# Performance work log

Measured on AMD Instinct MI355X. Metric: run time of the kernel, lower is better.

Reference implementation:

```python
import jax, jax.numpy as jnp
import numpy as np

N_NODES = 50000


def _gin_aggregate(x, src, dst):
    # sum_{j in N(i)} x_j via scatter-add over edges; eps=0 so add self term
    msg = x[src]  # [E, d]
    return x + jax.ops.segment_sum(msg, dst, num_segments=N_NODES)


def _mlp(h, Wa, ba, Wb, bb):
    return jax.nn.relu(h @ Wa + ba) @ Wb + bb


def setup_inputs() -> dict:
    key = jax.random.key(0)
    ks = jax.random.split(key, 12)
    d_in, d_h, n_cls, n_edges = 128, 128, 40, 800000
    x = jax.random.normal(ks[0], (N_NODES, d_in), dtype=jnp.float32)
    edge_index = jax.random.randint(ks[1], (2, n_edges), 0, N_NODES, dtype=jnp.int64)
    s = lambda k, sh: jax.random.normal(k, sh, dtype=jnp.float32) / np.sqrt(sh[0])
    return {
        "x": x,
        "edge_index": edge_index,
        "W11": s(ks[2], (d_in, 2 * d_h)), "b11": jnp.zeros((2 * d_h,), jnp.float32),
        "W12": s(ks[3], (2 * d_h, d_h)), "b12": jnp.zeros((d_h,), jnp.float32),
        "W21": s(ks[4], (d_h, 2 * d_h)), "b21": jnp.zeros((2 * d_h,), jnp.float32),
        "W22": s(ks[5], (2 * d_h, d_h)), "b22": jnp.zeros((d_h,), jnp.float32),
        "Wfc": s(ks[6], (d_h, n_cls)), "bfc": jnp.zeros((n_cls,), jnp.float32),
    }


def reference(x, edge_index, W11, b11, W12, b12, W21, b21, W22, b22, Wfc, bfc):
    src, dst = edge_index[0], edge_index[1]
    # GINConv 1: aggregate then MLP, followed by ReLU
    h = _mlp(_gin_aggregate(x, src, dst), W11, b11, W12, b12)
    h = jax.nn.relu(h)
    # GINConv 2
    h = _mlp(_gin_aggregate(h, src, dst), W21, b21, W22, b22)
    h = jax.nn.relu(h)
    # final classifier
    return h @ Wfc + bfc
```

## Files before the change

kernel.cpp:

```cpp
#include <hip/hip_runtime.h>

#define N_NODES 50000
#define N_EDGES 800000
#define NBUCK   98
#define EPB     8192
#define NSB     98
#define BCAP    160
#define CAPB    12288

typedef __attribute__((ext_vector_type(8))) short short8;
typedef __attribute__((ext_vector_type(4))) float floatx4;

__device__ __forceinline__ float b2f(unsigned short u) {
    union { unsigned int i; float f; } v;
    v.i = ((unsigned int)u) << 16;
    return v.f;
}
__device__ __forceinline__ float ubits(unsigned int b) {
    union { unsigned int i; float f; } v;
    v.i = b;
    return v.f;
}
__device__ __forceinline__ unsigned short f2b(float f) {
    union { float f; unsigned int i; } v;
    v.f = f;
    unsigned int r = v.i + 0x7FFFu + ((v.i >> 16) & 1u);
    return (unsigned short)(r >> 16);
}

__global__ __launch_bounds__(256) void prep_scatter(
    const float* __restrict__ x,
    const float* __restrict__ W11, const float* __restrict__ W12,
    const float* __restrict__ W21, const float* __restrict__ W22,
    const float* __restrict__ Wfc,
    const int* __restrict__ srcv, const int* __restrict__ dstv,
    unsigned short* __restrict__ xb,
    unsigned short* __restrict__ Wt11, unsigned short* __restrict__ Wt12,
    unsigned short* __restrict__ Wt21, unsigned short* __restrict__ Wt22,
    unsigned short* __restrict__ Wfct,
    int* __restrict__ cnt, int* __restrict__ tmp) {
    const int bid = blockIdx.x;
    const int tid = threadIdx.x;
    if (bid < 512) {
        int which = bid >> 7;
        int idx = (bid & 127) * 256 + tid;
        const float* W = (which == 0) ? W11 : (which == 1) ? W12 : (which == 2) ? W21 : W22;
        unsigned short* Wt = (which == 0) ? Wt11 : (which == 1) ? Wt12 : (which == 2) ? Wt21 : Wt22;
        int K = (which & 1) ? 256 : 128;
        int N = (which & 1) ? 128 : 256;
        int k = idx / N, n = idx - k * N;
        Wt[n * K + k] = f2b(W[idx]);
    } else if (bid < 536) {
        int idx = (bid - 512) * 256 + tid;
        int n = idx >> 7, k = idx & 127;
        Wfct[idx] = (n < 40) ? f2b(Wfc[k * 40 + n]) : (unsigned short)0;
    } else if (bid < 3661) {
        int i = (bid - 536) * 256 + tid;
        const float4 a = *reinterpret_cast<const float4*>(x + (size_t)i * 8);
        const float4 b = *reinterpret_cast<const float4*>(x + (size_t)i * 8 + 4);
        ushort4 u0, u1;
        u0.x = f2b(a.x); u0.y = f2b(a.y); u0.z = f2b(a.z); u0.w = f2b(a.w);
        u1.x = f2b(b.x); u1.y = f2b(b.y); u1.z = f2b(b.z); u1.w = f2b(b.w);
        *reinterpret_cast<ushort4*>(xb + (size_t)i * 8) = u0;
        *reinterpret_cast<ushort4*>(xb + (size_t)i * 8 + 4) = u1;
    } else {
        __shared__ int hist[NBUCK];
        const int k = bid - 3661;
        const int e0 = k * EPB;
        for (int i = tid; i < NBUCK; i += 256) hist[i] = 0;
        __syncthreads();
#pragma unroll 4
        for (int j = 0; j < EPB / 256; ++j) {
            int e = e0 + j * 256 + tid;
            if (e < N_EDGES) atomicAdd(&hist[dstv[e] >> 9], 1);
        }
        __syncthreads();
        for (int i = tid; i < NBUCK; i += 256) {
            cnt[i * NSB + k] = hist[i];
            hist[i] = 0;
        }
        __syncthreads();
#pragma unroll 4
        for (int j = 0; j < EPB / 256; ++j) {
            int e = e0 + j * 256 + tid;
            if (e < N_EDGES) {
                int d = dstv[e];
                int b = d >> 9;
                int r = atomicAdd(&hist[b], 1);
                if (r < BCAP)
                    tmp[((size_t)k * NBUCK + b) * BCAP + r] = srcv[e] | ((d & 511) << 16);
            }
        }
    }
}

__global__ __launch_bounds__(256) void bucket_sort_ex(const int* __restrict__ cnt,
                                                      const int* __restrict__ tmp,
                                                      int* __restrict__ e_src,
                                                      int* __restrict__ row_ptr) {
    __shared__ int ps[256];
    __shared__ int sb[NSB];
    __shared__ int sc[NSB];
    __shared__ int nc[512];
    __shared__ int buf[CAPB];
    const int tid = threadIdx.x;
    const int b = blockIdx.x;

    const int v = (tid < NSB) ? cnt[b * NSB + tid] : 0;
    ps[tid] = v;
    __syncthreads();
    for (int off = 1; off < 256; off <<= 1) {
        int u = (tid >= off) ? ps[tid - off] : 0;
        __syncthreads();
        ps[tid] += u;
        __syncthreads();
    }
    if (tid < NSB) {
        sb[tid] = ps[tid] - v;
        sc[tid] = v;
    }
    __syncthreads();
    const int S = ps[255];

    const int lane = tid & 63, w = tid >> 6;
    for (int k = w; k < NSB; k += 4) {
        const int base = sb[k], c = sc[k];
        const int* src = tmp + ((size_t)k * NBUCK + b) * BCAP;
        for (int i = lane; i < c; i += 64)
            if (base + i < CAPB) buf[base + i] = src[i];
    }
    for (int i = tid; i < 512; i += 256) nc[i] = 0;
    __syncthreads();
    for (int e = tid; e < S; e += 256)
        atomicAdd(&nc[(buf[e] >> 16) & 511], 1);
    __syncthreads();

    const int c0 = nc[2 * tid], c1 = nc[2 * tid + 1];
    ps[tid] = c0 + c1;
    __syncthreads();
    for (int off = 1; off < 256; off <<= 1) {
        int u = (tid >= off) ? ps[tid - off] : 0;
        __syncthreads();
        ps[tid] += u;
        __syncthreads();
    }
    const int off0 = ps[tid] - (c0 + c1);
    const int off1 = off0 + c0;
    nc[2 * tid] = off0;
    nc[2 * tid + 1] = off1;
    const int gbase = b * CAPB;
    row_ptr[b * 513 + 2 * tid] = gbase + off0;
    row_ptr[b * 513 + 2 * tid + 1] = gbase + off1;
    if (tid == 0) row_ptr[b * 513 + 512] = gbase + S;
    __syncthreads();

    for (int e = tid; e < S; e += 256) {
        int p = buf[e];
        int dl = (p >> 16) & 511;
        int pos = atomicAdd(&nc[dl], 1);
        e_src[gbase + pos] = p & 0xFFFF;
    }
}

__global__ __launch_bounds__(256) void agg_bf16q(const unsigned short* __restrict__ X,
                                                 const int* __restrict__ row_ptr,
                                                 const int* __restrict__ e_src,
                                                 unsigned short* __restrict__ agg) {
    const int node = (blockIdx.x * 256 + threadIdx.x) >> 6;
    const int lane = threadIdx.x & 63;
    const int qw = lane >> 4, ql = lane & 15;
    const size_t off = (size_t)ql * 8;

    const int rp = node + (node >> 9);
    const int beg = row_ptr[rp], end = row_ptr[rp + 1];
    float acc[8];
#pragma unroll
    for (int k = 0; k < 8; ++k) acc[k] = 0.f;

    if (qw == 0) {
        uint4 u = *reinterpret_cast<const uint4*>(X + (size_t)node * 128 + off);
        const unsigned int* up = (const unsigned int*)&u;
#pragma unroll
        for (int k = 0; k < 4; ++k) {
            acc[2 * k]     += ubits(up[k] << 16);
            acc[2 * k + 1] += ubits(up[k] & 0xFFFF0000u);
        }
    }

    int e = beg + qw;
    for (; e + 12 < end; e += 16) {
        const int s0 = e_src[e], s1 = e_src[e + 4], s2 = e_src[e + 8], s3 = e_src[e + 12];
        uint4 u0 = *reinterpret_cast<const uint4*>(X + (size_t)s0 * 128 + off);
        uint4 u1 = *reinterpret_cast<const uint4*>(X + (size_t)s1 * 128 + off);
        uint4 u2 = *reinterpret_cast<const uint4*>(X + (size_t)s2 * 128 + off);
        uint4 u3 = *reinterpret_cast<const uint4*>(X + (size_t)s3 * 128 + off);
        const unsigned int* p0 = (const unsigned int*)&u0;
        const unsigned int* p1 = (const unsigned int*)&u1;
        const unsigned int* p2 = (const unsigned int*)&u2;
        const unsigned int* p3 = (const unsigned int*)&u3;
#pragma unroll
        for (int k = 0; k < 4; ++k) {
            acc[2 * k]     += ubits(p0[k] << 16) + ubits(p1[k] << 16)
                            + ubits(p2[k] << 16) + ubits(p3[k] << 16);
            acc[2 * k + 1] += ubits(p0[k] & 0xFFFF0000u) + ubits(p1[k] & 0xFFFF0000u)
                            + ubits(p2[k] & 0xFFFF0000u) + ubits(p3[k] & 0xFFFF0000u);
        }
    }
    for (; e + 4 < end; e += 8) {
        const int s0 = e_src[e], s1 = e_src[e + 4];
        uint4 u0 = *reinterpret_cast<const uint4*>(X + (size_t)s0 * 128 + off);
        uint4 u1 = *reinterpret_cast<const uint4*>(X + (size_t)s1 * 128 + off);
        const unsigned int* p0 = (const unsigned int*)&u0;
        const unsigned int* p1 = (const unsigned int*)&u1;
#pragma unroll
        for (int k = 0; k < 4; ++k) {
            acc[2 * k]     += ubits(p0[k] << 16) + ubits(p1[k] << 16);
            acc[2 * k + 1] += ubits(p0[k] & 0xFFFF0000u) + ubits(p1[k] & 0xFFFF0000u);
        }
    }
    if (e < end) {
        const int s = e_src[e];
        uint4 u = *reinterpret_cast<const uint4*>(X + (size_t)s * 128 + off);
        const unsigned int* p = (const unsigned int*)&u;
#pragma unroll
        for (int k = 0; k < 4; ++k) {
            acc[2 * k]     += ubits(p[k] << 16);
            acc[2 * k + 1] += ubits(p[k] & 0xFFFF0000u);
        }
    }

#pragma unroll
    for (int k = 0; k < 8; ++k) acc[k] += __shfl_xor(acc[k], 32);
#pragma unroll
    for (int k = 0; k < 8; ++k) acc[k] += __shfl_xor(acc[k], 16);

    if (qw == 0) {
        ushort4 o0, o1;
        o0.x = f2b(acc[0]); o0.y = f2b(acc[1]); o0.z = f2b(acc[2]); o0.w = f2b(acc[3]);
        o1.x = f2b(acc[4]); o1.y = f2b(acc[5]); o1.z = f2b(acc[6]); o1.w = f2b(acc[7]);
        unsigned short* p = agg + (size_t)node * 128 + off;
        *reinterpret_cast<ushort4*>(p) = o0;
        *reinterpret_cast<ushort4*>(p + 4) = o1;
    }
}

template <bool FUSE>
__global__ __launch_bounds__(256, FUSE ? 2 : 3) void mlp_fused(
    const unsigned short* __restrict__ X, const unsigned short* __restrict__ Wt1,
    const float* __restrict__ b1, const unsigned short* __restrict__ Wt2,
    const float* __restrict__ b2, unsigned short* __restrict__ Y,
    const unsigned short* __restrict__ Wfct, const float* __restrict__ bfc,
    float* __restrict__ out, int M) {
    __shared__ __align__(16) char smem[FUSE ? 57344 : 52224];
    unsigned short* A   = (unsigned short*)smem;
    unsigned short* B2q = (unsigned short*)smem;
    unsigned short* B1h = (unsigned short*)(smem + 17408);
    unsigned short* T   = (unsigned short*)(smem + 17408);
    unsigned short* Hc  = (unsigned short*)(smem + 52224);

    const int tid = threadIdx.x;
    const int m0 = blockIdx.x * 64;
    const int lane = tid & 63, w = tid >> 6;
    const int qm = lane & 15, quad = lane >> 4;

#pragma unroll
    for (int j = 0; j < 4; ++j) {
        int i = j * 256 + tid;
        int r = i >> 4, c8 = (i & 15) << 3;
        uint4 v = {0, 0, 0, 0};
        if (m0 + r < M) v = *reinterpret_cast<const uint4*>(X + (size_t)(m0 + r) * 128 + c8);
        *reinterpret_cast<uint4*>(&A[r * 136 + c8]) = v;
    }

    floatx4 acc1[2][4][2];
#pragma unroll
    for (int c = 0; c < 2; ++c)
#pragma unroll
        for (int mt = 0; mt < 4; ++mt)
#pragma unroll
            for (int nt = 0; nt < 2; ++nt) acc1[c][mt][nt] = {0.f, 0.f, 0.f, 0.f};

    for (int c = 0; c < 2; ++c) {
#pragma unroll
        for (int j = 0; j < 8; ++j) {
            int i = j * 256 + tid;
            int r = i >> 4, c8 = (i & 15) << 3;
            *reinterpret_cast<uint4*>(&B1h[r * 136 + c8]) =
                *reinterpret_cast<const uint4*>(Wt1 + (size_t)(c * 128 + r) * 128 + c8);
        }
        __syncthreads();
#pragma unroll
        for (int ks = 0; ks < 4; ++ks) {
            const int kb = ks * 32 + quad * 8;
            short8 a[4], b[2];
#pragma unroll
            for (int mt = 0; mt < 4; ++mt)
                a[mt] = *reinterpret_cast<const short8*>(&A[(mt * 16 + qm) * 136 + kb]);
#pragma unroll
            for (int nt = 0; nt < 2; ++nt)
                b[nt] = *reinterpret_cast<const short8*>(&B1h[(w * 32 + nt * 16 + qm) * 136 + kb]);
#pragma unroll
            for (int mt = 0; mt < 4; ++mt)
#pragma unroll
                for (int nt = 0; nt < 2; ++nt)
                    acc1[c][mt][nt] = __builtin_amdgcn_mfma_f32_16x16x32_bf16(
                        a[mt], b[nt], acc1[c][mt][nt], 0, 0, 0);
        }
        __syncthreads();
    }

#pragma unroll
    for (int c = 0; c < 2; ++c) {
#pragma unroll
        for (int nt = 0; nt < 2; ++nt) {
            const int jcol = c * 128 + w * 32 + nt * 16 + qm;
            const float bj = b1[jcol];
#pragma unroll
            for (int mt = 0; mt < 4; ++mt)
#pragma unroll
                for (int r = 0; r < 4; ++r)
                    T[(mt * 16 + quad * 4 + r) * 264 + jcol] =
                        f2b(fmaxf(acc1[c][mt][nt][r] + bj, 0.f));
        }
    }

    floatx4 cacc[3];
#pragma unroll
    for (int nt = 0; nt < 3; ++nt) cacc[nt] = {0.f, 0.f, 0.f, 0.f};

    for (int c2 = 0; c2 < 4; ++c2) {
#pragma unroll
        for (int j = 0; j < 4; ++j) {
            int i = j * 256 + tid;
            int r = i >> 5, c8 = (i & 31) << 3;
            *reinterpret_cast<uint4*>(&B2q[r * 264 + c8]) =
                *reinterpret_cast<const uint4*>(Wt2 + (size_t)(c2 * 32 + r) * 256 + c8);
        }
        __syncthreads();

        floatx4 acc2[2];
        acc2[0] = {0.f, 0.f, 0.f, 0.f};
        acc2[1] = {0.f, 0.f, 0.f, 0.f};
#pragma unroll
        for (int ks = 0; ks < 8; ++ks) {
            const int kb = ks * 32 + quad * 8;
            short8 t0 = *reinterpret_cast<const short8*>(&T[((w & 1) * 32 + qm) * 264 + kb]);
            short8 t1 = *reinterpret_cast<const short8*>(&T[((w & 1) * 32 + 16 + qm) * 264 + kb]);
            short8 bb = *reinterpret_cast<const short8*>(&B2q[((w >> 1) * 16 + qm) * 264 + kb]);
            acc2[0] = __builtin_amdgcn_mfma_f32_16x16x32_bf16(t0, bb, acc2[0], 0, 0, 0);
            acc2[1] = __builtin_amdgcn_mfma_f32_16x16x32_bf16(t1, bb, acc2[1], 0, 0, 0);
        }

        const int ncol = c2 * 32 + (w >> 1) * 16 + qm;
        const float bj = b2[ncol];
        if (!FUSE) {
#pragma unroll
            for (int mt2 = 0; mt2 < 2; ++mt2)
#pragma unroll
                for (int r = 0; r < 4; ++r) {
                    int row = m0 + (w & 1) * 32 + mt2 * 16 + quad * 4 + r;
                    if (row < M)
                        Y[(size_t)row * 128 + ncol] = f2b(fmaxf(acc2[mt2][r] + bj, 0.f));
                }
            __syncthreads();
        } else {
            const int lcol = (w >> 1) * 16 + qm;
#pragma unroll
            for (int mt2 = 0; mt2 < 2; ++mt2)
#pragma unroll
                for (int r = 0; r < 4; ++r)
                    Hc[((w & 1) * 32 + mt2 * 16 + quad * 4 + r) * 40 + lcol] =
                        f2b(fmaxf(acc2[mt2][r] + bj, 0.f));
            __syncthreads();
            short8 hf = *reinterpret_cast<const short8*>(&Hc[(w * 16 + qm) * 40 + quad * 8]);
#pragma unroll
            for (int nt = 0; nt < 3; ++nt) {
                short8 bf = *reinterpret_cast<const short8*>(
                    Wfct + (nt * 16 + qm) * 128 + c2 * 32 + quad * 8);
                cacc[nt] = __builtin_amdgcn_mfma_f32_16x16x32_bf16(hf, bf, cacc[nt], 0, 0, 0);
            }
            __syncthreads();
        }
    }

    if (FUSE) {
#pragma unroll
        for (int nt = 0; nt < 3; ++nt) {
            int col = nt * 16 + qm;
            if (col < 40) {
                const float bj = bfc[col];
#pragma unroll
                for (int r = 0; r < 4; ++r) {
                    int row = m0 + w * 16 + quad * 4 + r;
                    if (row < M) out[(size_t)row * 40 + col] = cacc[nt][r] + bj;
                }
            }
        }
    }
}

extern "C" void kernel_launch(void* const* d_in, const int* in_sizes, int n_in,
                              void* d_out, int out_size, void* d_ws, size_t ws_size,
                              hipStream_t stream) {
    const float* x   = (const float*)d_in[0];
    const int*   ei  = (const int*)d_in[1];
    const float* W11 = (const float*)d_in[2];
    const float* b11 = (const float*)d_in[3];
    const float* W12 = (const float*)d_in[4];
    const float* b12 = (const float*)d_in[5];
    const float* W21 = (const float*)d_in[6];
    const float* b21 = (const float*)d_in[7];
    const float* W22 = (const float*)d_in[8];
    const float* b22 = (const float*)d_in[9];
    const float* Wfc = (const float*)d_in[10];
    const float* bfc = (const float*)d_in[11];
    float* out = (float*)d_out;

    const int* srcv = ei;
    const int* dstv = ei + N_EDGES;

    unsigned short* agg  = (unsigned short*)d_ws;
    unsigned short* h    = agg + (size_t)N_NODES * 128;
    unsigned short* xb   = h   + (size_t)N_NODES * 128;
    unsigned short* Wt11 = xb  + (size_t)N_NODES * 128;
    unsigned short* Wt12 = Wt11 + 256 * 128;
    unsigned short* Wt21 = Wt12 + 256 * 128;
    unsigned short* Wt22 = Wt21 + 256 * 128;
    unsigned short* Wfct = Wt22 + 256 * 128;
    int* cnt     = (int*)(Wfct + 48 * 128);
    int* row_ptr = cnt + 9728;
    int* e_src   = row_ptr + 50304;
    int* tmp     = e_src + (size_t)NBUCK * CAPB;

    prep_scatter<<<3661 + NSB, 256, 0, stream>>>(
        x, W11, W12, W21, W22, Wfc, srcv, dstv,
        xb, Wt11, Wt12, Wt21, Wt22, Wfct, cnt, tmp);

    bucket_sort_ex<<<NBUCK, 256, 0, stream>>>(cnt, tmp, e_src, row_ptr);

    const int agg_blocks = N_NODES * 64 / 256;
    const int mlp_blocks = (N_NODES + 63) / 64;

    agg_bf16q<<<agg_blocks, 256, 0, stream>>>(xb, row_ptr, e_src, agg);
    mlp_fused<false><<<mlp_blocks, 256, 0, stream>>>(
        agg, Wt11, b11, Wt12, b12, h, nullptr, nullptr, nullptr, N_NODES);
    agg_bf16q<<<agg_blocks, 256, 0, stream>>>(h, row_ptr, e_src, agg);
    mlp_fused<true><<<mlp_blocks, 256, 0, stream>>>(
        agg, Wt21, b21, Wt22, b22, nullptr, Wfct, bfc, out, N_NODES);
}
```

Baseline: 265.7 us.

## Split edge scatter into more smaller blocks and launch them first

Cuts edges per scatter block from 8192 to 2048, which raises the number of scatter blocks from 98 to 391 and shrinks the per-bucket capacity to 64. The scatter blocks are moved to the start of the prep grid so the long-running histogram work begins before the conversion blocks. The bucket sort now scans 391 source counts using a two-per-thread prefix sum and gathers with half-wavefronts. This adds more cnt storage, and with BCAP 64 any sub-bucket that overflows would silently drop edges.

```diff
diff --git a/kernel.cpp b/kernel.cpp
--- a/kernel.cpp
+++ b/kernel.cpp
@@ -3,9 +3,9 @@
 #define N_NODES 50000
 #define N_EDGES 800000
 #define NBUCK   98
-#define EPB     8192
-#define NSB     98
-#define BCAP    160
+#define EPB     2048
+#define NSB     391
+#define BCAP    64
 #define CAPB    12288
 
 typedef __attribute__((ext_vector_type(8))) short short8;
@@ -41,35 +41,13 @@
     int* __restrict__ cnt, int* __restrict__ tmp) {
     const int bid = blockIdx.x;
     const int tid = threadIdx.x;
-    if (bid < 512) {
-        int which = bid >> 7;
-        int idx = (bid & 127) * 256 + tid;
-        const float* W = (which == 0) ? W11 : (which == 1) ? W12 : (which == 2) ? W21 : W22;
-        unsigned short* Wt = (which == 0) ? Wt11 : (which == 1) ? Wt12 : (which == 2) ? Wt21 : Wt22;
-        int K = (which & 1) ? 256 : 128;
-        int N = (which & 1) ? 128 : 256;
-        int k = idx / N, n = idx - k * N;
-        Wt[n * K + k] = f2b(W[idx]);
-    } else if (bid < 536) {
-        int idx = (bid - 512) * 256 + tid;
-        int n = idx >> 7, k = idx & 127;
-        Wfct[idx] = (n < 40) ? f2b(Wfc[k * 40 + n]) : (unsigned short)0;
-    } else if (bid < 3661) {
-        int i = (bid - 536) * 256 + tid;
-        const float4 a = *reinterpret_cast<const float4*>(x + (size_t)i * 8);
-        const float4 b = *reinterpret_cast<const float4*>(x + (size_t)i * 8 + 4);
-        ushort4 u0, u1;
-        u0.x = f2b(a.x); u0.y = f2b(a.y); u0.z = f2b(a.z); u0.w = f2b(a.w);
-        u1.x = f2b(b.x); u1.y = f2b(b.y); u1.z = f2b(b.z); u1.w = f2b(b.w);
-        *reinterpret_cast<ushort4*>(xb + (size_t)i * 8) = u0;
-        *reinterpret_cast<ushort4*>(xb + (size_t)i * 8 + 4) = u1;
-    } else {
+    if (bid < NSB) {
         __shared__ int hist[NBUCK];
-        const int k = bid - 3661;
+        const int k = bid;
         const int e0 = k * EPB;
         for (int i = tid; i < NBUCK; i += 256) hist[i] = 0;
         __syncthreads();
-#pragma unroll 4
+#pragma unroll
         for (int j = 0; j < EPB / 256; ++j) {
             int e = e0 + j * 256 + tid;
             if (e < N_EDGES) atomicAdd(&hist[dstv[e] >> 9], 1);
@@ -80,7 +58,7 @@
             hist[i] = 0;
         }
         __syncthreads();
-#pragma unroll 4
+#pragma unroll
         for (int j = 0; j < EPB / 256; ++j) {
             int e = e0 + j * 256 + tid;
             if (e < N_EDGES) {
@@ -91,6 +69,29 @@
                     tmp[((size_t)k * NBUCK + b) * BCAP + r] = srcv[e] | ((d & 511) << 16);
             }
         }
+    } else if (bid < NSB + 512) {
+        int wb = bid - NSB;
+        int which = wb >> 7;
+        int idx = (wb & 127) * 256 + tid;
+        const float* W = (which == 0) ? W11 : (which == 1) ? W12 : (which == 2) ? W21 : W22;
+        unsigned short* Wt = (which == 0) ? Wt11 : (which == 1) ? Wt12 : (which == 2) ? Wt21 : Wt22;
+        int K = (which & 1) ? 256 : 128;
+        int N = (which & 1) ? 128 : 256;
+        int k = idx / N, n = idx - k * N;
+        Wt[n * K + k] = f2b(W[idx]);
+    } else if (bid < NSB + 536) {
+        int idx = (bid - NSB - 512) * 256 + tid;
+        int n = idx >> 7, k = idx & 127;
+        Wfct[idx] = (n < 40) ? f2b(Wfc[k * 40 + n]) : (unsigned short)0;
+    } else {
+        int i = (bid - NSB - 536) * 256 + tid;
+        const float4 a = *reinterpret_cast<const float4*>(x + (size_t)i * 8);
+        const float4 b = *reinterpret_cast<const float4*>(x + (size_t)i * 8 + 4);
+        ushort4 u0, u1;
+        u0.x = f2b(a.x); u0.y = f2b(a.y); u0.z = f2b(a.z); u0.w = f2b(a.w);
+        u1.x = f2b(b.x); u1.y = f2b(b.y); u1.z = f2b(b.z); u1.w = f2b(b.w);
+        *reinterpret_cast<ushort4*>(xb + (size_t)i * 8) = u0;
+        *reinterpret_cast<ushort4*>(xb + (size_t)i * 8 + 4) = u1;
     }
 }
 
@@ -99,15 +100,18 @@
                                                       int* __restrict__ e_src,
                                                       int* __restrict__ row_ptr) {
     __shared__ int ps[256];
-    __shared__ int sb[NSB];
-    __shared__ int sc[NSB];
+    __shared__ int sb[512];
+    __shared__ int sc[512];
     __shared__ int nc[512];
     __shared__ int buf[CAPB];
     const int tid = threadIdx.x;
     const int b = blockIdx.x;
 
-    const int v = (tid < NSB) ? cnt[b * NSB + tid] : 0;
-    ps[tid] = v;
+    sc[tid] = (tid < NSB) ? cnt[b * NSB + tid] : 0;
+    sc[tid + 256] = (tid + 256 < NSB) ? cnt[b * NSB + tid + 256] : 0;
+    __syncthreads();
+    const int c0s = sc[2 * tid], c1s = sc[2 * tid + 1];
+    ps[tid] = c0s + c1s;
     __syncthreads();
     for (int off = 1; off < 256; off <<= 1) {
         int u = (tid >= off) ? ps[tid - off] : 0;
@@ -115,18 +119,18 @@
         ps[tid] += u;
         __syncthreads();
     }
-    if (tid < NSB) {
-        sb[tid] = ps[tid] - v;
-        sc[tid] = v;
-    }
+    const int soff0 = ps[tid] - (c0s + c1s);
+    sb[2 * tid] = soff0;
+    sb[2 * tid + 1] = soff0 + c0s;
     __syncthreads();
     const int S = ps[255];
 
     const int lane = tid & 63, w = tid >> 6;
-    for (int k = w; k < NSB; k += 4) {
+    const int hw = w * 2 + (lane >> 5), hl = lane & 31;
+    for (int k = hw; k < NSB; k += 8) {
         const int base = sb[k], c = sc[k];
         const int* src = tmp + ((size_t)k * NBUCK + b) * BCAP;
-        for (int i = lane; i < c; i += 64)
+        for (int i = hl; i < c; i += 32)
             if (base + i < CAPB) buf[base + i] = src[i];
     }
     for (int i = tid; i < 512; i += 256) nc[i] = 0;
@@ -428,11 +432,11 @@
     unsigned short* Wt22 = Wt21 + 256 * 128;
     unsigned short* Wfct = Wt22 + 256 * 128;
     int* cnt     = (int*)(Wfct + 48 * 128);
-    int* row_ptr = cnt + 9728;
+    int* row_ptr = cnt + 38400;
     int* e_src   = row_ptr + 50304;
     int* tmp     = e_src + (size_t)NBUCK * CAPB;
 
-    prep_scatter<<<3661 + NSB, 256, 0, stream>>>(
+    prep_scatter<<<NSB + 3661, 256, 0, stream>>>(
         x, W11, W12, W21, W22, Wfc, srcv, dstv,
         xb, Wt11, Wt12, Wt21, Wt22, Wfct, cnt, tmp);
 
```

New measurement: 245.6 us, median of 2. 7.5% less time.
